# Kernel tuning notes

Hardware: AMD Instinct MI355X
Metric: run time of the kernel (lower is better)

## Reference

```python
import jax, jax.numpy as jnp
import numpy as np

EPS = 1e-12  # matches torch F.normalize eps


def setup_inputs() -> dict:
    key = jax.random.key(0)
    k_x, k_w, k_b, k_c, k_f = jax.random.split(key, 5)
    N, C, H, W = 32, 128, 64, 64
    K = 64
    x = jax.random.normal(k_x, (N, C, H, W), dtype=jnp.float32)
    conv_w = jax.random.normal(k_w, (K, C), dtype=jnp.float32) * 0.05  # 1x1 conv weight [K,C,1,1] squeezed
    conv_b = jax.random.normal(k_b, (K,), dtype=jnp.float32) * 0.05
    centroids = jax.random.uniform(k_c, (K, C), dtype=jnp.float32)
    fc_w = jax.random.normal(k_f, (1, K), dtype=jnp.float32) * 0.1  # nn.Linear(K,1,bias=False).weight
    return {"x": x, "conv_w": conv_w, "conv_b": conv_b, "centroids": centroids, "fc_w": fc_w}


def _l2norm(v, axis):
    return v / jnp.maximum(jnp.linalg.norm(v, axis=axis, keepdims=True), EPS)


def reference(x, conv_w, conv_b, centroids, fc_w):
    N, C, H, W = x.shape
    K = conv_w.shape[0]
    # descriptor-wise L2 normalize over channel dim
    x = _l2norm(x, axis=1)
    xf = x.reshape(N, C, H * W)                                   # [N,C,S]
    # 1x1 conv == per-pixel linear over channels
    logits = jnp.einsum('kc,ncs->nks', conv_w, xf) + conv_b[None, :, None]
    a = jax.nn.softmax(logits, axis=1)                            # [N,K,S] soft assignment
    # VLAD: sum_s a[n,k,s] * (x[n,:,s] - centroids[k,:]), loop-free
    vlad = jnp.einsum('nks,ncs->nkc', a, xf) \
           - a.sum(axis=-1)[..., None] * centroids[None, :, :]    # [N,K,C]
    # intra-normalization over descriptor dim
    vlad = _l2norm(vlad, axis=2)
    # lastfc: [N,C,K] @ [K] -> [N,C]
    out = jnp.einsum('nkc,k->nc', vlad, fc_w[0])
    return out
```

## Files before the change

### kernel.cpp

```cpp
#include <hip/hip_runtime.h>
#include <math.h>

#define Nn 32
#define Cc 128
#define Ss 4096
#define Kk 64
#define NCHUNK 16
#define SCHUNK (Ss / NCHUNK)
#define ST 64
#define NSUB (SCHUNK / ST)
#define BLK 256

#define XCS 72
#define XTS 136
#define LKS 68
#define AS  72
#define RS  17

typedef __attribute__((ext_vector_type(8))) short short8;
typedef __attribute__((ext_vector_type(4))) float float4v;

__device__ __forceinline__ unsigned f2bf(float f) {
    unsigned u = __builtin_bit_cast(unsigned, f);
    return (u + 0x7fffu + ((u >> 16) & 1u)) >> 16;
}
__device__ __forceinline__ unsigned pack2(float a, float b) {
    return f2bf(a) | (f2bf(b) << 16);
}

__device__ __forceinline__ void bar_lds() {
    asm volatile("s_waitcnt lgkmcnt(0)" ::: "memory");
    __builtin_amdgcn_s_barrier();
    asm volatile("" ::: "memory");
}

__global__ __launch_bounds__(BLK, 2) void netvlad_main(
    const float* __restrict__ x,
    const float* __restrict__ conv_w,
    const float* __restrict__ conv_b,
    float* __restrict__ vladp,
    float* __restrict__ asump,
    float* __restrict__ out)
{
    __shared__ __align__(16) unsigned short xC[Cc * XCS];
    __shared__ __align__(16) float Lbuf[ST * LKS];
    __shared__ __align__(16) unsigned short aB[Kk * AS];
    __shared__ float red[ST * RS];
    __shared__ float invn[ST];
    unsigned short* xT = (unsigned short*)Lbuf;

    const int t     = threadIdx.x;
    const int n     = blockIdx.y;
    const int chunk = blockIdx.x;
    const int w    = t >> 6;
    const int l    = t & 63;
    const int m    = l & 15;
    const int quad = l >> 4;
    const int p    = t >> 2;
    const int ii   = t & 3;

    if (chunk == 0 && n == 0) {
        float4 z4 = make_float4(0.f, 0.f, 0.f, 0.f);
#pragma unroll
        for (int i = 0; i < 4; ++i)
            ((float4*)out)[t + 256 * i] = z4;
    }

    short8 wfrag[4];
    {
        const float* wr_ = conv_w + (16 * w + m) * Cc;
#pragma unroll
        for (int ks = 0; ks < 4; ++ks) {
            float4 wa = *(const float4*)(wr_ + 32 * ks + 8 * quad);
            float4 wb = *(const float4*)(wr_ + 32 * ks + 8 * quad + 4);
            union { short8 s8; unsigned u[4]; } W_;
            W_.u[0] = pack2(wa.x, wa.y);
            W_.u[1] = pack2(wa.z, wa.w);
            W_.u[2] = pack2(wb.x, wb.y);
            W_.u[3] = pack2(wb.z, wb.w);
            wfrag[ks] = W_.s8;
        }
    }
    float bias_r[4];
#pragma unroll
    for (int r = 0; r < 4; ++r) bias_r[r] = conv_b[16 * w + 4 * quad + r];

    float4v acc[8];
#pragma unroll
    for (int nt = 0; nt < 8; ++nt) acc[nt] = (float4v){0.f, 0.f, 0.f, 0.f};
    float asum_part[16];
#pragma unroll
    for (int j = 0; j < 16; ++j) asum_part[j] = 0.f;

    const float* xn = x + (size_t)n * Cc * Ss;

    const int sq   = (t & 15) << 2;
    const int crow = t >> 4;
    const float* xbase = xn + (size_t)crow * Ss + chunk * SCHUNK + sq;
    float4 pf[8];
#pragma unroll
    for (int r = 0; r < 8; ++r)
        pf[r] = *(const float4*)(xbase + (size_t)(16 * r) * Ss);

    for (int sub = 0; sub < NSUB; ++sub) {
        bar_lds();

        {
            float sp0 = 0.f, sp1 = 0.f, sp2 = 0.f, sp3 = 0.f;
#pragma unroll
            for (int r = 0; r < 8; ++r) {
                float4 v = pf[r];
                sp0 += v.x * v.x; sp1 += v.y * v.y;
                sp2 += v.z * v.z; sp3 += v.w * v.w;
                uint2 pk = make_uint2(pack2(v.x, v.y), pack2(v.z, v.w));
                *(uint2*)&xC[(crow + 16 * r) * XCS + sq] = pk;
            }
            red[(sq + 0) * RS + crow] = sp0;
            red[(sq + 1) * RS + crow] = sp1;
            red[(sq + 2) * RS + crow] = sp2;
            red[(sq + 3) * RS + crow] = sp3;
        }
        if (sub < NSUB - 1) {
#pragma unroll
            for (int r = 0; r < 8; ++r)
                pf[r] = *(const float4*)(xbase + (size_t)(16 * r) * Ss + (sub + 1) * ST);
        }
        bar_lds();

        if (t < ST) {
            float tot = 0.f;
#pragma unroll
            for (int i = 0; i < 16; ++i) tot += red[t * RS + i];
            invn[t] = 1.0f / fmaxf(sqrtf(tot), 1e-12f);
        }
        {
            int s = t & 63, oct0 = t >> 6;
#pragma unroll
            for (int q = 0; q < 4; ++q) {
                int oct = oct0 + 4 * q;
                uint4 dd;
                dd.x = (unsigned)xC[(8 * oct + 0) * XCS + s] | ((unsigned)xC[(8 * oct + 1) * XCS + s] << 16);
                dd.y = (unsigned)xC[(8 * oct + 2) * XCS + s] | ((unsigned)xC[(8 * oct + 3) * XCS + s] << 16);
                dd.z = (unsigned)xC[(8 * oct + 4) * XCS + s] | ((unsigned)xC[(8 * oct + 5) * XCS + s] << 16);
                dd.w = (unsigned)xC[(8 * oct + 6) * XCS + s] | ((unsigned)xC[(8 * oct + 7) * XCS + s] << 16);
                *(uint4*)&xT[s * XTS + 8 * oct] = dd;
            }
        }
        bar_lds();

        float4v Lr[4];
#pragma unroll
        for (int nt = 0; nt < 4; ++nt) Lr[nt] = (float4v){0.f, 0.f, 0.f, 0.f};
#pragma unroll
        for (int nt = 0; nt < 4; ++nt) {
#pragma unroll
            for (int ks = 0; ks < 4; ++ks) {
                short8 b = *(const short8*)&xT[(16 * nt + m) * XTS + 32 * ks + 8 * quad];
                Lr[nt] = __builtin_amdgcn_mfma_f32_16x16x32_bf16(wfrag[ks], b, Lr[nt], 0, 0, 0);
            }
        }
        bar_lds();

#pragma unroll
        for (int nt = 0; nt < 4; ++nt) {
            float iv = invn[16 * nt + m];
            float4 o;
            o.x = Lr[nt].x * iv + bias_r[0];
            o.y = Lr[nt].y * iv + bias_r[1];
            o.z = Lr[nt].z * iv + bias_r[2];
            o.w = Lr[nt].w * iv + bias_r[3];
            *(float4*)&Lbuf[(16 * nt + m) * LKS + 16 * w + 4 * quad] = o;
        }
        bar_lds();

        {
            float lv[16];
#pragma unroll
            for (int j = 0; j < 16; ++j) lv[j] = Lbuf[p * LKS + ii + 4 * j];
            float mx = lv[0];
#pragma unroll
            for (int j = 1; j < 16; ++j) mx = fmaxf(mx, lv[j]);
            mx = fmaxf(mx, __shfl_xor(mx, 1));
            mx = fmaxf(mx, __shfl_xor(mx, 2));
            float e[16];
            float lsum = 0.f;
#pragma unroll
            for (int j = 0; j < 16; ++j) { e[j] = __expf(lv[j] - mx); lsum += e[j]; }
            lsum += __shfl_xor(lsum, 1);
            lsum += __shfl_xor(lsum, 2);
            float itot = 1.0f / lsum;
            float sca  = itot * invn[p];
#pragma unroll
            for (int j = 0; j < 16; ++j) {
                float av = e[j] * itot;
                asum_part[j] += av;
                aB[(ii + 4 * j) * AS + p] = (unsigned short)f2bf(e[j] * sca);
            }
        }
        bar_lds();

#pragma unroll
        for (int ks = 0; ks < 2; ++ks) {
            short8 af = *(const short8*)&aB[(16 * w + m) * AS + 32 * ks + 8 * quad];
#pragma unroll
            for (int nt = 0; nt < 8; ++nt) {
                short8 bf_ = *(const short8*)&xC[(16 * nt + m) * XCS + 32 * ks + 8 * quad];
                acc[nt] = __builtin_amdgcn_mfma_f32_16x16x32_bf16(af, bf_, acc[nt], 0, 0, 0);
            }
        }
    }

    {
        float* vb = vladp + ((((size_t)chunk * Nn + n) * Kk) + 16 * w + 4 * quad) * Cc + m;
#pragma unroll
        for (int nt = 0; nt < 8; ++nt) {
            vb[0 * Cc + 16 * nt] = acc[nt].x;
            vb[1 * Cc + 16 * nt] = acc[nt].y;
            vb[2 * Cc + 16 * nt] = acc[nt].z;
            vb[3 * Cc + 16 * nt] = acc[nt].w;
        }
    }

    __syncthreads();
#pragma unroll
    for (int j = 0; j < 16; ++j) Lbuf[p * LKS + ii + 4 * j] = asum_part[j];
    __syncthreads();
    if (t < Kk) {
        float s_ = 0.f;
        for (int p2 = 0; p2 < ST; ++p2) s_ += Lbuf[p2 * LKS + t];
        asump[((size_t)chunk * Nn + n) * Kk + t] = s_;
    }
}

__global__ __launch_bounds__(BLK) void netvlad_final(
    const float* __restrict__ vladp,
    const float* __restrict__ asump,
    const float* __restrict__ centroids,
    const float* __restrict__ fc_w,
    float* __restrict__ out)
{
    __shared__ float asum_s[8];
    __shared__ float scale_s[8];
    __shared__ float4 osum[8 * 32];

    const int t   = threadIdx.x;
    const int bid = blockIdx.x;
    const int n2  = bid >> 3;
    const int kg  = bid & 7;
    const int kl  = t >> 5;
    const int c4  = t & 31;
    const int k2  = 8 * kg + kl;

    float4 v = make_float4(0.f, 0.f, 0.f, 0.f);
    const float* vp = vladp + ((size_t)n2 * Kk + k2) * Cc + 4 * c4;
#pragma unroll
    for (int ch = 0; ch < NCHUNK; ++ch) {
        float4 u = *(const float4*)(vp + (size_t)ch * Nn * Kk * Cc);
        v.x += u.x; v.y += u.y; v.z += u.z; v.w += u.w;
    }
    if (t < 8) {
        float a = 0.f;
#pragma unroll
        for (int ch = 0; ch < NCHUNK; ++ch)
            a += asump[((size_t)ch * Nn + n2) * Kk + 8 * kg + t];
        asum_s[t] = a;
    }
    __syncthreads();

    const float a2 = asum_s[kl];
    float4 cv = *(const float4*)(centroids + (size_t)k2 * Cc + 4 * c4);
    float dx = v.x - a2 * cv.x;
    float dy = v.y - a2 * cv.y;
    float dz = v.z - a2 * cv.z;
    float dw = v.w - a2 * cv.w;

    float ssq = dx * dx + dy * dy + dz * dz + dw * dw;
    ssq += __shfl_xor(ssq, 1);
    ssq += __shfl_xor(ssq, 2);
    ssq += __shfl_xor(ssq, 4);
    ssq += __shfl_xor(ssq, 8);
    ssq += __shfl_xor(ssq, 16);
    if ((t & 31) == 0)
        scale_s[kl] = fc_w[k2] / fmaxf(sqrtf(ssq), 1e-12f);
    __syncthreads();

    const float sc = scale_s[kl];
    osum[kl * 32 + c4] = make_float4(sc * dx, sc * dy, sc * dz, sc * dw);
    __syncthreads();

    if (t < 32) {
        float4 tot = osum[t];
#pragma unroll
        for (int kl2 = 1; kl2 < 8; ++kl2) {
            float4 o2 = osum[kl2 * 32 + t];
            tot.x += o2.x; tot.y += o2.y; tot.z += o2.z; tot.w += o2.w;
        }
        atomicAdd(&out[n2 * Cc + 4 * t + 0], tot.x);
        atomicAdd(&out[n2 * Cc + 4 * t + 1], tot.y);
        atomicAdd(&out[n2 * Cc + 4 * t + 2], tot.z);
        atomicAdd(&out[n2 * Cc + 4 * t + 3], tot.w);
    }
}

extern "C" void kernel_launch(void* const* d_in, const int* in_sizes, int n_in,
                              void* d_out, int out_size, void* d_ws, size_t ws_size,
                              hipStream_t stream) {
    (void)in_sizes; (void)n_in; (void)out_size; (void)ws_size;
    const float* x         = (const float*)d_in[0];
    const float* conv_w    = (const float*)d_in[1];
    const float* conv_b    = (const float*)d_in[2];
    const float* centroids = (const float*)d_in[3];
    const float* fc_w      = (const float*)d_in[4];
    float* out = (float*)d_out;

    float* vladp = (float*)d_ws;
    float* asump = vladp + (size_t)NCHUNK * Nn * Kk * Cc;

    dim3 grid(NCHUNK, Nn);
    netvlad_main<<<grid, BLK, 0, stream>>>(x, conv_w, conv_b, vladp, asump, out);
    netvlad_final<<<dim3(Nn * 8), BLK, 0, stream>>>(vladp, asump, centroids, fc_w, out);
}
```

Measured before the change: 113.8 us.

## Fuse the LDS transpose into the load phase and raise chunk count and occupancy

Each thread now loads 8 consecutive channels instead of channels strided by 16. That lets it write both the channel-major xC tile and the transposed xT tile straight from registers, which removes the separate LDS read-back transpose pass and one block barrier per sub-tile. The spatial chunk count doubles to 32, giving more blocks. The launch bound asks for 3 blocks per SIMD, which adds parallelism but may force register spills and doubles the partial-result reduction work.

Result: slower. 123.7 us (+8.7%).

```diff
diff --git a/kernel.cpp b/kernel.cpp
--- a/kernel.cpp
+++ b/kernel.cpp
@@ -5,7 +5,7 @@
 #define Cc 128
 #define Ss 4096
 #define Kk 64
-#define NCHUNK 16
+#define NCHUNK 32
 #define SCHUNK (Ss / NCHUNK)
 #define ST 64
 #define NSUB (SCHUNK / ST)
@@ -24,9 +24,6 @@
     unsigned u = __builtin_bit_cast(unsigned, f);
     return (u + 0x7fffu + ((u >> 16) & 1u)) >> 16;
 }
-__device__ __forceinline__ unsigned pack2(float a, float b) {
-    return f2bf(a) | (f2bf(b) << 16);
-}
 
 __device__ __forceinline__ void bar_lds() {
     asm volatile("s_waitcnt lgkmcnt(0)" ::: "memory");
@@ -34,7 +31,7 @@
     asm volatile("" ::: "memory");
 }
 
-__global__ __launch_bounds__(BLK, 2) void netvlad_main(
+__global__ __launch_bounds__(BLK, 3) void netvlad_main(
     const float* __restrict__ x,
     const float* __restrict__ conv_w,
     const float* __restrict__ conv_b,
@@ -74,10 +71,10 @@
             float4 wa = *(const float4*)(wr_ + 32 * ks + 8 * quad);
             float4 wb = *(const float4*)(wr_ + 32 * ks + 8 * quad + 4);
             union { short8 s8; unsigned u[4]; } W_;
-            W_.u[0] = pack2(wa.x, wa.y);
-            W_.u[1] = pack2(wa.z, wa.w);
-            W_.u[2] = pack2(wb.x, wb.y);
-            W_.u[3] = pack2(wb.z, wb.w);
+            W_.u[0] = f2bf(wa.x) | (f2bf(wa.y) << 16);
+            W_.u[1] = f2bf(wa.z) | (f2bf(wa.w) << 16);
+            W_.u[2] = f2bf(wb.x) | (f2bf(wb.y) << 16);
+            W_.u[3] = f2bf(wb.z) | (f2bf(wb.w) << 16);
             wfrag[ks] = W_.s8;
         }
     }
@@ -96,24 +93,40 @@
 
     const int sq   = (t & 15) << 2;
     const int crow = t >> 4;
-    const float* xbase = xn + (size_t)crow * Ss + chunk * SCHUNK + sq;
+    const float* xbase = xn + (size_t)(8 * crow) * Ss + chunk * SCHUNK + sq;
     float4 pf[8];
 #pragma unroll
     for (int r = 0; r < 8; ++r)
-        pf[r] = *(const float4*)(xbase + (size_t)(16 * r) * Ss);
+        pf[r] = *(const float4*)(xbase + (size_t)r * Ss);
 
     for (int sub = 0; sub < NSUB; ++sub) {
         bar_lds();
 
         {
+            unsigned bf[8][4];
             float sp0 = 0.f, sp1 = 0.f, sp2 = 0.f, sp3 = 0.f;
 #pragma unroll
             for (int r = 0; r < 8; ++r) {
                 float4 v = pf[r];
                 sp0 += v.x * v.x; sp1 += v.y * v.y;
                 sp2 += v.z * v.z; sp3 += v.w * v.w;
-                uint2 pk = make_uint2(pack2(v.x, v.y), pack2(v.z, v.w));
-                *(uint2*)&xC[(crow + 16 * r) * XCS + sq] = pk;
+                bf[r][0] = f2bf(v.x); bf[r][1] = f2bf(v.y);
+                bf[r][2] = f2bf(v.z); bf[r][3] = f2bf(v.w);
+            }
+#pragma unroll
+            for (int r = 0; r < 8; ++r) {
+                uint2 pk = make_uint2(bf[r][0] | (bf[r][1] << 16),
+                                      bf[r][2] | (bf[r][3] << 16));
+                *(uint2*)&xC[(8 * crow + r) * XCS + sq] = pk;
+            }
+#pragma unroll
+            for (int i = 0; i < 4; ++i) {
+                uint4 dd;
+                dd.x = bf[0][i] | (bf[1][i] << 16);
+                dd.y = bf[2][i] | (bf[3][i] << 16);
+                dd.z = bf[4][i] | (bf[5][i] << 16);
+                dd.w = bf[6][i] | (bf[7][i] << 16);
+                *(uint4*)&xT[(sq + i) * XTS + 8 * crow] = dd;
             }
             red[(sq + 0) * RS + crow] = sp0;
             red[(sq + 1) * RS + crow] = sp1;
@@ -123,7 +136,7 @@
         if (sub < NSUB - 1) {
 #pragma unroll
             for (int r = 0; r < 8; ++r)
-                pf[r] = *(const float4*)(xbase + (size_t)(16 * r) * Ss + (sub + 1) * ST);
+                pf[r] = *(const float4*)(xbase + (size_t)r * Ss + (sub + 1) * ST);
         }
         bar_lds();
 
@@ -133,21 +146,6 @@
             for (int i = 0; i < 16; ++i) tot += red[t * RS + i];
             invn[t] = 1.0f / fmaxf(sqrtf(tot), 1e-12f);
         }
-        {
-            int s = t & 63, oct0 = t >> 6;
-#pragma unroll
-            for (int q = 0; q < 4; ++q) {
-                int oct = oct0 + 4 * q;
-                uint4 dd;
-                dd.x = (unsigned)xC[(8 * oct + 0) * XCS + s] | ((unsigned)xC[(8 * oct + 1) * XCS + s] << 16);
-                dd.y = (unsigned)xC[(8 * oct + 2) * XCS + s] | ((unsigned)xC[(8 * oct + 3) * XCS + s] << 16);
-                dd.z = (unsigned)xC[(8 * oct + 4) * XCS + s] | ((unsigned)xC[(8 * oct + 5) * XCS + s] << 16);
-                dd.w = (unsigned)xC[(8 * oct + 6) * XCS + s] | ((unsigned)xC[(8 * oct + 7) * XCS + s] << 16);
-                *(uint4*)&xT[s * XTS + 8 * oct] = dd;
-            }
-        }
-        bar_lds();
-
         float4v Lr[4];
 #pragma unroll
         for (int nt = 0; nt < 4; ++nt) Lr[nt] = (float4v){0.f, 0.f, 0.f, 0.f};
```
